# Performance work log

Hardware: AMD Instinct MI355X
Metric: run time of the kernel (lower is better)

Reference implementation:

```python
import jax, jax.numpy as jnp
import numpy as np

B, D, PRE, NEXT, SC, ANT = 1000, 8, 98, 512, 32, 5  # batch, devices, split-in, split-out, subcarriers, antennas
TAU = 0.1  # noise std (tau2 in original torch.normal(0, tau2, ...))


def setup_inputs() -> dict:
    key = jax.random.key(0)
    ks = jax.random.split(key, 18)
    rn = lambda k, s, sc=0.05: (jax.random.normal(k, s, jnp.float32) * sc)
    return {
        "x": jax.random.normal(ks[0], (B, D * PRE), jnp.float32),
        "noise": jax.random.normal(ks[1], (B, SC, ANT), jnp.float32) * TAU,
        "sub_w": rn(ks[2], (D, PRE, NEXT)),
        "sub_b": rn(ks[3], (D, NEXT)),
        "ln_gamma": jnp.ones((D, NEXT), jnp.float32),
        "ln_beta": jnp.zeros((D, NEXT), jnp.float32),
        "cut_w": rn(ks[4], (D, NEXT, SC)),
        "cut_b": rn(ks[5], (D, SC)),
        "b_mat": rn(ks[6], (D, SC), 1.0),
        "h_mat": rn(ks[7], (D, SC, ANT), 1.0),
        "a_mat": rn(ks[8], (SC, ANT), 1.0),
        "cut_layer_bias": rn(ks[9], (SC,)),
        "fc3_w": rn(ks[10], (SC, 98)),
        "fc3_b": rn(ks[11], (98,)),
        "fc4_w": rn(ks[12], (98, 49)),
        "fc4_b": rn(ks[13], (49,)),
        "out_w": rn(ks[14], (49, 10)),
        "out_b": rn(ks[15], (10,)),
        "k_idx": jax.random.permutation(ks[16], SC).astype(jnp.int32),  # one-hot indicator_mat as index map
    }


def reference(x, noise, sub_w, sub_b, ln_gamma, ln_beta, cut_w, cut_b,
              b_mat, h_mat, a_mat, cut_layer_bias,
              fc3_w, fc3_b, fc4_w, fc4_b, out_w, out_b, k_idx):
    # split x into per-device chunks: torch.split along dim=1 with uniform sizes
    xs = x.reshape(B, D, PRE).transpose(1, 0, 2)                       # (D, B, PRE)
    h = jax.nn.relu(jnp.einsum('dbi,dio->dbo', xs, sub_w) + sub_b[:, None, :])
    mu = jnp.mean(h, axis=-1, keepdims=True)
    var = jnp.mean(jnp.square(h - mu), axis=-1, keepdims=True)
    h = (h - mu) * jax.lax.rsqrt(var + 1e-5) * ln_gamma[:, None, :] + ln_beta[:, None, :]
    cut = jax.nn.relu(jnp.einsum('dbo,doc->dbc', h, cut_w) + cut_b[:, None, :])  # (D, B, SC)
    # h_vec[n, j] = a_j^T h_mat[n, k(j)]  (indicator one-hot -> gather)
    h_sel = h_mat[:, k_idx, :]                                         # (D, SC, ANT)
    h_vec = jnp.einsum('dkc,kc->dk', h_sel, a_mat)                     # (D, SC)
    # received = sum_n (cut_n * b_n) * h_vec_n
    received = jnp.einsum('dbc,dc,dc->bc', cut, b_mat, h_vec)          # (B, SC)
    scaled_noise = jnp.einsum('bjc,jc->bj', noise, a_mat)              # (B, SC)
    z = jax.nn.relu(received + scaled_noise + cut_layer_bias)
    z = jax.nn.relu(z @ fc3_w + fc3_b)
    z = jax.nn.relu(z @ fc4_w + fc4_b)
    return jax.nn.log_softmax(z @ out_w + out_b, axis=1)
```

## Files before the change

kernel.cpp:

```cpp
#include <hip/hip_runtime.h>
#include <math.h>

#define B 1000
#define D 8
#define PRE 98
#define NEXT 512
#define SC 32
#define ANT 5
#define BM 32
#define NTILE 32
#define KP 128
#define CSTRIDE 32

#define OW3 0
#define OW4 3136
#define OWO 7938
#define OB3 8428
#define OB4 8526
#define OBO 8575
#define WTOT 8585

using bf16x8 = __attribute__((ext_vector_type(8))) short;
using f32x4  = __attribute__((ext_vector_type(4))) float;

static __device__ __forceinline__ unsigned short f2bf(float f) {
    union { float f; unsigned u; } v{f};
    unsigned r = (v.u + 0x7fffu + ((v.u >> 16) & 1u)) >> 16;
    return (unsigned short)r;
}
static __device__ __forceinline__ float bf2f(unsigned short h) {
    union { unsigned u; float f; } v{(unsigned)h << 16};
    return v.f;
}

__global__ __launch_bounds__(256) void k_prep(const float* __restrict__ sub_w,
                                              const float* __restrict__ cut_w,
                                              unsigned short* __restrict__ sub_wT,
                                              unsigned short* __restrict__ cut_wT,
                                              int* __restrict__ counters) {
    __shared__ __align__(16) unsigned short tile[32][128];
    int t = threadIdx.x, bid = blockIdx.x;
    if (bid == 0 && t < NTILE)
        __hip_atomic_store(&counters[t * CSTRIDE], 0, __ATOMIC_RELAXED,
                           __HIP_MEMORY_SCOPE_AGENT);
    if (bid < 128) {
        int d = bid >> 4, n0 = (bid & 15) * 32;
        int nn = t & 31, kk = t >> 5;
#pragma unroll
        for (int j = 0; j < 16; ++j) {
            int k = j * 8 + kk;
            float v = (k < PRE) ? sub_w[(d * PRE + k) * NEXT + n0 + nn] : 0.f;
            tile[nn][k] = f2bf(v);
        }
        __syncthreads();
        int row = t >> 3, c0 = (t & 7) * 16;
        unsigned short* dst = sub_wT + ((size_t)(d * NEXT + n0 + row)) * KP + c0;
        *reinterpret_cast<bf16x8*>(dst)     = *reinterpret_cast<bf16x8*>(&tile[row][c0]);
        *reinterpret_cast<bf16x8*>(dst + 8) = *reinterpret_cast<bf16x8*>(&tile[row][c0 + 8]);
    } else {
        int bb = bid - 128;
        int d = bb >> 2, k0 = (bb & 3) * 128;
        int nn = t & 31, kk = t >> 5;
#pragma unroll
        for (int j = 0; j < 16; ++j) {
            int kl = j * 8 + kk;
            tile[nn][kl] = f2bf(cut_w[(d * NEXT + k0 + kl) * SC + nn]);
        }
        __syncthreads();
        int row = t >> 3, c0 = (t & 7) * 16;
        unsigned short* dst = cut_wT + ((size_t)(d * SC + row)) * NEXT + k0 + c0;
        *reinterpret_cast<bf16x8*>(dst)     = *reinterpret_cast<bf16x8*>(&tile[row][c0]);
        *reinterpret_cast<bf16x8*>(dst + 8) = *reinterpret_cast<bf16x8*>(&tile[row][c0 + 8]);
    }
}

__global__ __launch_bounds__(512) void k_all(const float* __restrict__ x,
                                             const unsigned short* __restrict__ sub_wT,
                                             const float* __restrict__ sub_b,
                                             const float* __restrict__ gamma,
                                             const float* __restrict__ beta,
                                             const unsigned short* __restrict__ cut_wT,
                                             const float* __restrict__ cut_b,
                                             const float* __restrict__ b_mat,
                                             const float* __restrict__ h_mat,
                                             const float* __restrict__ a_mat,
                                             const int* __restrict__ k_idx,
                                             const float* __restrict__ noise,
                                             const float* __restrict__ clb,
                                             const float* __restrict__ fc3_w,
                                             const float* __restrict__ fc3_b,
                                             const float* __restrict__ fc4_w,
                                             const float* __restrict__ fc4_b,
                                             const float* __restrict__ out_w,
                                             const float* __restrict__ out_b,
                                             float* __restrict__ part,
                                             int* __restrict__ counters,
                                             float* __restrict__ out) {
    __shared__ __align__(16) unsigned short x_lds[BM][136];
    __shared__ __align__(16) unsigned short h_lds[BM][536];
    __shared__ float W_lds[WTOT];
    __shared__ float clb_s[SC], am_s[SC * ANT];
    __shared__ float z_s[4][SC];
    __shared__ float z3_s[4][98];
    __shared__ float z4_s[4][49];

    int t = threadIdx.x;
    int d = blockIdx.x >> 5;
    int tile = blockIdx.x & 31;
    int b0 = tile * BM;
    int w = t >> 6, lane = t & 63;
    int lr = lane >> 4, lc = lane & 15;

    int n0 = w * 64;
    const unsigned short* bw = sub_wT + (size_t)d * NEXT * KP + (size_t)(n0 + lc) * KP + lr * 8;
    bf16x8 bq[4][4];
#pragma unroll
    for (int ks = 0; ks < 4; ++ks)
#pragma unroll
        for (int nf = 0; nf < 4; ++nf)
            bq[ks][nf] = *reinterpret_cast<const bf16x8*>(bw + (size_t)nf * 16 * KP + ks * 32);

    for (int idx = t; idx < BM * 136; idx += 512) {
        int r = idx / 136, i = idx - r * 136;
        int b = b0 + r;
        float v = (b < B && i < PRE) ? x[b * (D * PRE) + d * PRE + i] : 0.f;
        x_lds[r][i] = f2bf(v);
    }
    __syncthreads();

    f32x4 acc[2][4] = {};
#pragma unroll
    for (int ks = 0; ks < 4; ++ks) {
        bf16x8 a0 = *reinterpret_cast<const bf16x8*>(&x_lds[lc][ks * 32 + lr * 8]);
        bf16x8 a1 = *reinterpret_cast<const bf16x8*>(&x_lds[16 + lc][ks * 32 + lr * 8]);
#pragma unroll
        for (int nf = 0; nf < 4; ++nf) {
            acc[0][nf] = __builtin_amdgcn_mfma_f32_16x16x32_bf16(a0, bq[ks][nf], acc[0][nf], 0, 0, 0);
            acc[1][nf] = __builtin_amdgcn_mfma_f32_16x16x32_bf16(a1, bq[ks][nf], acc[1][nf], 0, 0, 0);
        }
    }

    bf16x8 gq[16];
    float cf = 0.f, cb = 0.f;
    if (w < 4) {
        int nt = w & 1;
        const unsigned short* cw = cut_wT + (size_t)(d * SC + nt * 16 + lc) * NEXT + lr * 8;
#pragma unroll
        for (int ks = 0; ks < 16; ++ks)
            gq[ks] = *reinterpret_cast<const bf16x8*>(cw + ks * 32);
        int c = nt * 16 + lc;
        int kk = k_idx[c];
        float hv = 0.f;
#pragma unroll
        for (int a = 0; a < ANT; ++a)
            hv = fmaf(h_mat[(d * SC + kk) * ANT + a], a_mat[c * ANT + a], hv);
        cf = b_mat[d * SC + c] * hv;
        cb = cut_b[d * SC + c];
    }

    {
        const float* sb = sub_b + d * NEXT;
#pragma unroll
        for (int nf = 0; nf < 4; ++nf) {
            int n = n0 + nf * 16 + lc;
            float bias = sb[n];
#pragma unroll
            for (int mt = 0; mt < 2; ++mt)
#pragma unroll
                for (int r = 0; r < 4; ++r)
                    h_lds[mt * 16 + lr * 4 + r][n] = f2bf(fmaxf(acc[mt][nf][r] + bias, 0.f));
        }
    }
    __syncthreads();

    {
        int row = t >> 4, l16 = t & 15;
        unsigned int* hrow = reinterpret_cast<unsigned int*>(&h_lds[row][0]);
        float s1 = 0.f, s2 = 0.f;
#pragma unroll
        for (int j = 0; j < 16; ++j) {
            unsigned int p = hrow[l16 + j * 16];
            float v0 = bf2f((unsigned short)(p & 0xffffu));
            float v1 = bf2f((unsigned short)(p >> 16));
            s1 += v0 + v1;
            s2 += v0 * v0 + v1 * v1;
        }
#pragma unroll
        for (int off = 8; off >= 1; off >>= 1) {
            s1 += __shfl_xor(s1, off, 16);
            s2 += __shfl_xor(s2, off, 16);
        }
        float mu = s1 * (1.f / NEXT);
        float var = s2 * (1.f / NEXT) - mu * mu;
        float rs = rsqrtf(var + 1e-5f);
        const float* g = gamma + d * NEXT;
        const float* be = beta + d * NEXT;
#pragma unroll
        for (int j = 0; j < 16; ++j) {
            int pi = l16 + j * 16;
            unsigned int p = hrow[pi];
            int n = pi * 2;
            float v0 = (bf2f((unsigned short)(p & 0xffffu)) - mu) * rs * g[n] + be[n];
            float v1 = (bf2f((unsigned short)(p >> 16)) - mu) * rs * g[n + 1] + be[n + 1];
            hrow[pi] = (unsigned)f2bf(v0) | ((unsigned)f2bf(v1) << 16);
        }
    }
    __syncthreads();

    if (w < 4) {
        int mt = w >> 1, nt = w & 1;
        f32x4 acc2 = {};
#pragma unroll
        for (int ks = 0; ks < 16; ++ks) {
            bf16x8 a = *reinterpret_cast<const bf16x8*>(&h_lds[mt * 16 + lc][ks * 32 + lr * 8]);
            acc2 = __builtin_amdgcn_mfma_f32_16x16x32_bf16(a, gq[ks], acc2, 0, 0, 0);
        }
        int c = nt * 16 + lc;
#pragma unroll
        for (int r = 0; r < 4; ++r) {
            int m = mt * 16 + lr * 4 + r;
            int b = b0 + m;
            if (b < B)
                __hip_atomic_store(&part[((size_t)b * D + d) * SC + c],
                                   fmaxf(acc2[r] + cb, 0.f) * cf,
                                   __ATOMIC_RELAXED, __HIP_MEMORY_SCOPE_AGENT);
        }
    } else {
        int tt = t - 256;
        for (int i = tt; i < 3136; i += 256) W_lds[OW3 + i] = fc3_w[i];
        for (int i = tt; i < 4802; i += 256) W_lds[OW4 + i] = fc4_w[i];
        for (int i = tt; i < 490; i += 256)  W_lds[OWO + i] = out_w[i];
        if (tt < 98) W_lds[OB3 + tt] = fc3_b[tt];
        if (tt < 49) W_lds[OB4 + tt] = fc4_b[tt];
        if (tt < 10) W_lds[OBO + tt] = out_b[tt];
        if (tt >= 128 && tt < 128 + SC) clb_s[tt - 128] = clb[tt - 128];
        if (tt >= 160 && tt < 160 + SC * ANT) am_s[tt - 160] = a_mat[tt - 160];
    }

    __syncthreads();
    if (t == 0) {
        __hip_atomic_fetch_add(&counters[tile * CSTRIDE], 1,
                               __ATOMIC_RELAXED, __HIP_MEMORY_SCOPE_AGENT);
        while (__hip_atomic_load(&counters[tile * CSTRIDE],
                                 __ATOMIC_RELAXED, __HIP_MEMORY_SCOPE_AGENT) < D)
            __builtin_amdgcn_s_sleep(2);
    }
    __syncthreads();

    if (w < 4) {
        int b = b0 + d * 4 + w;
        if (b < B) {
            int c = lane & 31, dg = lane >> 5;
            float s = 0.f;
#pragma unroll
            for (int i = 0; i < 4; ++i)
                s += __hip_atomic_load(&part[((size_t)b * D + (dg + 2 * i)) * SC + c],
                                       __ATOMIC_RELAXED, __HIP_MEMORY_SCOPE_AGENT);
            s += __shfl_xor(s, 32);
            if (lane < 32) {
                float zz = s + clb_s[c];
#pragma unroll
                for (int a = 0; a < ANT; ++a)
                    zz = fmaf(noise[(b * SC + c) * ANT + a], am_s[c * ANT + a], zz);
                z_s[w][c] = fmaxf(zz, 0.f);
            }
            for (int o = lane; o < 98; o += 64) {
                float s3 = W_lds[OB3 + o];
#pragma unroll
                for (int j = 0; j < SC; ++j) s3 = fmaf(z_s[w][j], W_lds[OW3 + j * 98 + o], s3);
                z3_s[w][o] = fmaxf(s3, 0.f);
            }
            if (lane < 49) {
                float s4 = W_lds[OB4 + lane];
                for (int j = 0; j < 98; ++j) s4 = fmaf(z3_s[w][j], W_lds[OW4 + j * 49 + lane], s4);
                z4_s[w][lane] = fmaxf(s4, 0.f);
            }
            float v = -INFINITY;
            if (lane < 10) {
                float so = W_lds[OBO + lane];
                for (int j = 0; j < 49; ++j) so = fmaf(z4_s[w][j], W_lds[OWO + j * 10 + lane], so);
                v = so;
            }
            float mx = v;
#pragma unroll
            for (int off = 8; off >= 1; off >>= 1) mx = fmaxf(mx, __shfl_xor(mx, off, 16));
            float e = (lane < 10) ? expf(v - mx) : 0.f;
            float ssum = e;
#pragma unroll
            for (int off = 8; off >= 1; off >>= 1) ssum += __shfl_xor(ssum, off, 16);
            if (lane < 10) out[b * 10 + lane] = v - mx - logf(ssum);
        }
    }
}

extern "C" void kernel_launch(void* const* d_in, const int* in_sizes, int n_in,
                              void* d_out, int out_size, void* d_ws, size_t ws_size,
                              hipStream_t stream) {
    const float* x      = (const float*)d_in[0];
    const float* noise  = (const float*)d_in[1];
    const float* sub_w  = (const float*)d_in[2];
    const float* sub_b  = (const float*)d_in[3];
    const float* ln_g   = (const float*)d_in[4];
    const float* ln_b   = (const float*)d_in[5];
    const float* cut_w  = (const float*)d_in[6];
    const float* cut_b  = (const float*)d_in[7];
    const float* b_mat  = (const float*)d_in[8];
    const float* h_mat  = (const float*)d_in[9];
    const float* a_mat  = (const float*)d_in[10];
    const float* clb    = (const float*)d_in[11];
    const float* fc3_w  = (const float*)d_in[12];
    const float* fc3_b  = (const float*)d_in[13];
    const float* fc4_w  = (const float*)d_in[14];
    const float* fc4_b  = (const float*)d_in[15];
    const float* out_w  = (const float*)d_in[16];
    const float* out_b  = (const float*)d_in[17];
    const int*   k_idx  = (const int*)d_in[18];
    float* out = (float*)d_out;

    char* ws = (char*)d_ws;
    float* part            = (float*)ws;
    unsigned short* sub_wT = (unsigned short*)(ws + (1 << 20));
    unsigned short* cut_wT = (unsigned short*)(ws + (2 << 20));
    int* counters          = (int*)(ws + (2 << 20) + (1 << 18));

    k_prep<<<160, 256, 0, stream>>>(sub_w, cut_w, sub_wT, cut_wT, counters);
    k_all<<<D * NTILE, 512, 0, stream>>>(x, sub_wT, sub_b, ln_g, ln_b, cut_wT,
                                         cut_b, b_mat, h_mat, a_mat, k_idx,
                                         noise, clb, fc3_w, fc3_b, fc4_w,
                                         fc4_b, out_w, out_b, part, counters,
                                         out);
}
```

Baseline: 28.90 us.

## Fold LayerNorm affine into cut weights and fuse statistics into GEMM epilogue

LayerNorm is rewritten algebraically: gamma is folded into the transposed cut weights, and the per-column sums of gamma*W and beta*W plus cut_b are precomputed in the prep kernel. The main kernel now gathers row mean and variance from the first GEMM's accumulators with shuffles and an LDS reduction, so the separate normalization pass over h_lds and one barrier are removed. The h-vector coefficient is also moved into prep, and x is loaded straight into registers instead of staging through LDS. The trade-off is that un-normalized bf16 activations feed the second GEMM, so precision changes, and x loads become per-lane scalar reads.

```diff
diff --git a/kernel.cpp b/kernel.cpp
--- a/kernel.cpp
+++ b/kernel.cpp
@@ -28,17 +28,24 @@
     unsigned r = (v.u + 0x7fffu + ((v.u >> 16) & 1u)) >> 16;
     return (unsigned short)r;
 }
-static __device__ __forceinline__ float bf2f(unsigned short h) {
-    union { unsigned u; float f; } v{(unsigned)h << 16};
-    return v.f;
-}
 
 __global__ __launch_bounds__(256) void k_prep(const float* __restrict__ sub_w,
                                               const float* __restrict__ cut_w,
+                                              const float* __restrict__ gamma,
+                                              const float* __restrict__ beta,
+                                              const float* __restrict__ cut_b,
+                                              const float* __restrict__ b_mat,
+                                              const float* __restrict__ h_mat,
+                                              const float* __restrict__ a_mat,
+                                              const int* __restrict__ k_idx,
                                               unsigned short* __restrict__ sub_wT,
                                               unsigned short* __restrict__ cut_wT,
+                                              float* __restrict__ gwsum,
+                                              float* __restrict__ bwv,
+                                              float* __restrict__ coef,
                                               int* __restrict__ counters) {
     __shared__ __align__(16) unsigned short tile[32][128];
+    __shared__ float gs_l[8][32], bs_l[8][32];
     int t = threadIdx.x, bid = blockIdx.x;
     if (bid == 0 && t < NTILE)
         __hip_atomic_store(&counters[t * CSTRIDE], 0, __ATOMIC_RELAXED,
@@ -58,46 +65,57 @@
         *reinterpret_cast<bf16x8*>(dst)     = *reinterpret_cast<bf16x8*>(&tile[row][c0]);
         *reinterpret_cast<bf16x8*>(dst + 8) = *reinterpret_cast<bf16x8*>(&tile[row][c0 + 8]);
     } else {
-        int bb = bid - 128;
-        int d = bb >> 2, k0 = (bb & 3) * 128;
-        int nn = t & 31, kk = t >> 5;
-#pragma unroll
-        for (int j = 0; j < 16; ++j) {
-            int kl = j * 8 + kk;
-            tile[nn][kl] = f2bf(cut_w[(d * NEXT + k0 + kl) * SC + nn]);
-        }
+        int d = bid - 128;
+        int c = t & 31, ko = t >> 5;
+        float gs = 0.f, bs = 0.f;
+        for (int kk = ko; kk < NEXT; kk += 8) {
+            float wv = cut_w[(size_t)(d * NEXT + kk) * SC + c];
+            float g  = gamma[d * NEXT + kk];
+            float be = beta[d * NEXT + kk];
+            cut_wT[(size_t)(d * SC + c) * NEXT + kk] = f2bf(g * wv);
+            gs += g * wv;
+            bs += be * wv;
+        }
+        gs_l[ko][c] = gs;
+        bs_l[ko][c] = bs;
         __syncthreads();
-        int row = t >> 3, c0 = (t & 7) * 16;
-        unsigned short* dst = cut_wT + ((size_t)(d * SC + row)) * NEXT + k0 + c0;
-        *reinterpret_cast<bf16x8*>(dst)     = *reinterpret_cast<bf16x8*>(&tile[row][c0]);
-        *reinterpret_cast<bf16x8*>(dst + 8) = *reinterpret_cast<bf16x8*>(&tile[row][c0 + 8]);
+        if (t < SC) {
+            float G = 0.f, Bb = 0.f;
+#pragma unroll
+            for (int j = 0; j < 8; ++j) { G += gs_l[j][t]; Bb += bs_l[j][t]; }
+            gwsum[d * SC + t] = G;
+            bwv[d * SC + t] = Bb + cut_b[d * SC + t];
+            int kk = k_idx[t];
+            float hv = 0.f;
+#pragma unroll
+            for (int a = 0; a < ANT; ++a)
+                hv = fmaf(h_mat[(d * SC + kk) * ANT + a], a_mat[t * ANT + a], hv);
+            coef[d * SC + t] = b_mat[d * SC + t] * hv;
+        }
     }
 }
 
-__global__ __launch_bounds__(512) void k_all(const float* __restrict__ x,
-                                             const unsigned short* __restrict__ sub_wT,
-                                             const float* __restrict__ sub_b,
-                                             const float* __restrict__ gamma,
-                                             const float* __restrict__ beta,
-                                             const unsigned short* __restrict__ cut_wT,
-                                             const float* __restrict__ cut_b,
-                                             const float* __restrict__ b_mat,
-                                             const float* __restrict__ h_mat,
-                                             const float* __restrict__ a_mat,
-                                             const int* __restrict__ k_idx,
-                                             const float* __restrict__ noise,
-                                             const float* __restrict__ clb,
-                                             const float* __restrict__ fc3_w,
-                                             const float* __restrict__ fc3_b,
-                                             const float* __restrict__ fc4_w,
-                                             const float* __restrict__ fc4_b,
-                                             const float* __restrict__ out_w,
-                                             const float* __restrict__ out_b,
-                                             float* __restrict__ part,
-                                             int* __restrict__ counters,
-                                             float* __restrict__ out) {
-    __shared__ __align__(16) unsigned short x_lds[BM][136];
+__global__ __launch_bounds__(512) void k_main(const float* __restrict__ x,
+                                              const unsigned short* __restrict__ sub_wT,
+                                              const float* __restrict__ sub_b,
+                                              const unsigned short* __restrict__ cut_wT,
+                                              const float* __restrict__ gwsum,
+                                              const float* __restrict__ bwv,
+                                              const float* __restrict__ coef,
+                                              const float* __restrict__ noise,
+                                              const float* __restrict__ clb,
+                                              const float* __restrict__ a_mat,
+                                              const float* __restrict__ fc3_w,
+                                              const float* __restrict__ fc3_b,
+                                              const float* __restrict__ fc4_w,
+                                              const float* __restrict__ fc4_b,
+                                              const float* __restrict__ out_w,
+                                              const float* __restrict__ out_b,
+                                              float* __restrict__ part,
+                                              int* __restrict__ counters,
+                                              float* __restrict__ out) {
     __shared__ __align__(16) unsigned short h_lds[BM][536];
+    __shared__ __align__(16) float st_l[BM][2][8];
     __shared__ float W_lds[WTOT];
     __shared__ float clb_s[SC], am_s[SC * ANT];
     __shared__ float z_s[4][SC];
@@ -110,119 +128,118 @@
     int b0 = tile * BM;
     int w = t >> 6, lane = t & 63;
     int lr = lane >> 4, lc = lane & 15;
-
     int n0 = w * 64;
-    const unsigned short* bw = sub_wT + (size_t)d * NEXT * KP + (size_t)(n0 + lc) * KP + lr * 8;
+
+    bf16x8 af[2][4];
+#pragma unroll
+    for (int mt = 0; mt < 2; ++mt) {
+        int row = b0 + mt * 16 + lc;
+        bool ok = row < B;
+        const float* xr = x + (size_t)(ok ? row : 0) * (D * PRE) + d * PRE;
+#pragma unroll
+        for (int ks = 0; ks < 4; ++ks) {
+            int k0 = ks * 32 + lr * 8;
+            bf16x8 v;
+#pragma unroll
+            for (int j = 0; j < 8; ++j) {
+                int k = k0 + j;
+                float f = (ok && k < PRE) ? xr[k] : 0.f;
+                v[j] = (short)f2bf(f);
+            }
+            af[mt][ks] = v;
+        }
+    }
+
+    const unsigned short* bwp = sub_wT + (size_t)d * NEXT * KP + (size_t)(n0 + lc) * KP + lr * 8;
     bf16x8 bq[4][4];
 #pragma unroll
     for (int ks = 0; ks < 4; ++ks)
 #pragma unroll
         for (int nf = 0; nf < 4; ++nf)
-            bq[ks][nf] = *reinterpret_cast<const bf16x8*>(bw + (size_t)nf * 16 * KP + ks * 32);
-
-    for (int idx = t; idx < BM * 136; idx += 512) {
-        int r = idx / 136, i = idx - r * 136;
-        int b = b0 + r;
-        float v = (b < B && i < PRE) ? x[b * (D * PRE) + d * PRE + i] : 0.f;
-        x_lds[r][i] = f2bf(v);
-    }
-    __syncthreads();
-
-    f32x4 acc[2][4] = {};
-#pragma unroll
-    for (int ks = 0; ks < 4; ++ks) {
-        bf16x8 a0 = *reinterpret_cast<const bf16x8*>(&x_lds[lc][ks * 32 + lr * 8]);
-        bf16x8 a1 = *reinterpret_cast<const bf16x8*>(&x_lds[16 + lc][ks * 32 + lr * 8]);
-#pragma unroll
-        for (int nf = 0; nf < 4; ++nf) {
-            acc[0][nf] = __builtin_amdgcn_mfma_f32_16x16x32_bf16(a0, bq[ks][nf], acc[0][nf], 0, 0, 0);
-            acc[1][nf] = __builtin_amdgcn_mfma_f32_16x16x32_bf16(a1, bq[ks][nf], acc[1][nf], 0, 0, 0);
-        }
-    }
+            bq[ks][nf] = *reinterpret_cast<const bf16x8*>(bwp + (size_t)nf * 16 * KP + ks * 32);
+
+    float bias[4];
+#pragma unroll
+    for (int nf = 0; nf < 4; ++nf) bias[nf] = sub_b[d * NEXT + n0 + nf * 16 + lc];
 
     bf16x8 gq[16];
-    float cf = 0.f, cb = 0.f;
+    float gw_c = 0.f, bw_c = 0.f, cf_c = 0.f;
     if (w < 4) {
-        int nt = w & 1;
-        const unsigned short* cw = cut_wT + (size_t)(d * SC + nt * 16 + lc) * NEXT + lr * 8;
+        int c = (w & 1) * 16 + lc;
+        const unsigned short* cw = cut_wT + (size_t)(d * SC + c) * NEXT + lr * 8;
 #pragma unroll
         for (int ks = 0; ks < 16; ++ks)
             gq[ks] = *reinterpret_cast<const bf16x8*>(cw + ks * 32);
-        int c = nt * 16 + lc;
-        int kk = k_idx[c];
-        float hv = 0.f;
-#pragma unroll
-        for (int a = 0; a < ANT; ++a)
-            hv = fmaf(h_mat[(d * SC + kk) * ANT + a], a_mat[c * ANT + a], hv);
-        cf = b_mat[d * SC + c] * hv;
-        cb = cut_b[d * SC + c];
-    }
-
-    {
-        const float* sb = sub_b + d * NEXT;
+        gw_c = gwsum[d * SC + c];
+        bw_c = bwv[d * SC + c];
+        cf_c = coef[d * SC + c];
+    }
+
+    f32x4 acc[2][4] = {};
+#pragma unroll
+    for (int ks = 0; ks < 4; ++ks)
 #pragma unroll
         for (int nf = 0; nf < 4; ++nf) {
-            int n = n0 + nf * 16 + lc;
-            float bias = sb[n];
-#pragma unroll
-            for (int mt = 0; mt < 2; ++mt)
-#pragma unroll
-                for (int r = 0; r < 4; ++r)
-                    h_lds[mt * 16 + lr * 4 + r][n] = f2bf(fmaxf(acc[mt][nf][r] + bias, 0.f));
-        }
-    }
+            acc[0][nf] = __builtin_amdgcn_mfma_f32_16x16x32_bf16(af[0][ks], bq[ks][nf], acc[0][nf], 0, 0, 0);
+            acc[1][nf] = __builtin_amdgcn_mfma_f32_16x16x32_bf16(af[1][ks], bq[ks][nf], acc[1][nf], 0, 0, 0);
+        }
+
+    float s1[2][4] = {}, s2[2][4] = {};
+#pragma unroll
+    for (int nf = 0; nf < 4; ++nf) {
+        int n = n0 + nf * 16 + lc;
+#pragma unroll
+        for (int mt = 0; mt < 2; ++mt)
+#pragma unroll
+            for (int r = 0; r < 4; ++r) {
+                float hv = fmaxf(acc[mt][nf][r] + bias[nf], 0.f);
+                h_lds[mt * 16 + lr * 4 + r][n] = f2bf(hv);
+                s1[mt][r] += hv;
+                s2[mt][r] += hv * hv;
+            }
+    }
+#pragma unroll
+    for (int mt = 0; mt < 2; ++mt)
+#pragma unroll
+        for (int r = 0; r < 4; ++r) {
+#pragma unroll
+            for (int off = 8; off >= 1; off >>= 1) {
+                s1[mt][r] += __shfl_xor(s1[mt][r], off, 16);
+                s2[mt][r] += __shfl_xor(s2[mt][r], off, 16);
+            }
+            if (lc == 0) {
+                int row = mt * 16 + lr * 4 + r;
+                st_l[row][0][w] = s1[mt][r];
+                st_l[row][1][w] = s2[mt][r];
+            }
+        }
     __syncthreads();
 
-    {
-        int row = t >> 4, l16 = t & 15;
-        unsigned int* hrow = reinterpret_cast<unsigned int*>(&h_lds[row][0]);
-        float s1 = 0.f, s2 = 0.f;
-#pragma unroll
-        for (int j = 0; j < 16; ++j) {
-            unsigned int p = hrow[l16 + j * 16];
-            float v0 = bf2f((unsigned short)(p & 0xffffu));
-            float v1 = bf2f((unsigned short)(p >> 16));
-            s1 += v0 + v1;
-            s2 += v0 * v0 + v1 * v1;
-        }
-#pragma unroll
-        for (int off = 8; off >= 1; off >>= 1) {
-            s1 += __shfl_xor(s1, off, 16);
-            s2 += __shfl_xor(s2, off, 16);
-        }
-        float mu = s1 * (1.f / NEXT);
-        float var = s2 * (1.f / NEXT) - mu * mu;
-        float rs = rsqrtf(var + 1e-5f);
-        const float* g = gamma + d * NEXT;
-        const float* be = beta + d * NEXT;
-#pragma unroll
-        for (int j = 0; j < 16; ++j) {
-            int pi = l16 + j * 16;
-            unsigned int p = hrow[pi];
-            int n = pi * 2;
-            float v0 = (bf2f((unsigned short)(p & 0xffffu)) - mu) * rs * g[n] + be[n];
-            float v1 = (bf2f((unsigned short)(p >> 16)) - mu) * rs * g[n + 1] + be[n + 1];
-            hrow[pi] = (unsigned)f2bf(v0) | ((unsigned)f2bf(v1) << 16);
-        }
-    }
-    __syncthreads();
-
     if (w < 4) {
-        int mt = w >> 1, nt = w & 1;
-        f32x4 acc2 = {};
+        int mt = w >> 1;
+        int c = (w & 1) * 16 + lc;
+        f32x4 a2 = {};
 #pragma unroll
         for (int ks = 0; ks < 16; ++ks) {
             bf16x8 a = *reinterpret_cast<const bf16x8*>(&h_lds[mt * 16 + lc][ks * 32 + lr * 8]);
-            acc2 = __builtin_amdgcn_mfma_f32_16x16x32_bf16(a, gq[ks], acc2, 0, 0, 0);
-        }
-        int c = nt * 16 + lc;
+            a2 = __builtin_amdgcn_mfma_f32_16x16x32_bf16(a, gq[ks], a2, 0, 0, 0);
+        }
 #pragma unroll
         for (int r = 0; r < 4; ++r) {
             int m = mt * 16 + lr * 4 + r;
             int b = b0 + m;
+            float4 sa = *reinterpret_cast<const float4*>(&st_l[m][0][0]);
+            float4 sb = *reinterpret_cast<const float4*>(&st_l[m][0][4]);
+            float4 qa = *reinterpret_cast<const float4*>(&st_l[m][1][0]);
+            float4 qb = *reinterpret_cast<const float4*>(&st_l[m][1][4]);
+            float S1 = (sa.x + sa.y) + (sa.z + sa.w) + (sb.x + sb.y) + (sb.z + sb.w);
+            float S2 = (qa.x + qa.y) + (qa.z + qa.w) + (qb.x + qb.y) + (qb.z + qb.w);
+            float mu = S1 * (1.f / NEXT);
+            float var = S2 * (1.f / NEXT) - mu * mu;
+            float rs = rsqrtf(var + 1e-5f);
+            float cutv = fmaxf(rs * (a2[r] - mu * gw_c) + bw_c, 0.f) * cf_c;
             if (b < B)
-                __hip_atomic_store(&part[((size_t)b * D + d) * SC + c],
-                                   fmaxf(acc2[r] + cb, 0.f) * cf,
+                __hip_atomic_store(&part[((size_t)b * D + d) * SC + c], cutv,
                                    __ATOMIC_RELAXED, __HIP_MEMORY_SCOPE_AGENT);
         }
     } else {
@@ -321,12 +338,16 @@
     float* part            = (float*)ws;
     unsigned short* sub_wT = (unsigned short*)(ws + (1 << 20));
     unsigned short* cut_wT = (unsigned short*)(ws + (2 << 20));
-    int* counters          = (int*)(ws + (2 << 20) + (1 << 18));
-
-    k_prep<<<160, 256, 0, stream>>>(sub_w, cut_w, sub_wT, cut_wT, counters);
-    k_all<<<D * NTILE, 512, 0, stream>>>(x, sub_wT, sub_b, ln_g, ln_b, cut_wT,
-                                         cut_b, b_mat, h_mat, a_mat, k_idx,
-                                         noise, clb, fc3_w, fc3_b, fc4_w,
-                                         fc4_b, out_w, out_b, part, counters,
-                                         out);
+    float* gwsum           = (float*)(ws + (2 << 20) + 262144);
+    float* bwv             = (float*)(ws + (2 << 20) + 263168);
+    float* coef            = (float*)(ws + (2 << 20) + 264192);
+    int* counters          = (int*)(ws + (2 << 20) + 266240);
+
+    k_prep<<<136, 256, 0, stream>>>(sub_w, cut_w, ln_g, ln_b, cut_b, b_mat,
+                                    h_mat, a_mat, k_idx, sub_wT, cut_wT,
+                                    gwsum, bwv, coef, counters);
+    k_main<<<D * NTILE, 512, 0, stream>>>(x, sub_wT, sub_b, cut_wT, gwsum, bwv,
+                                          coef, noise, clb, a_mat, fc3_w, fc3_b,
+                                          fc4_w, fc4_b, out_w, out_b, part,
+                                          counters, out);
 }
```

New measurement: 49.60 us. 71.6% more time.
